# Kernel tuning notes

Hardware: AMD Instinct MI355X
Metric: run time of the kernel (lower is better)

## Reference

```python
import jax, jax.numpy as jnp
import numpy as np

D_MODEL = 1024
D_HIDDEN = 4096
N_EXPERTS = 8
N_TOKENS = 4096


def setup_inputs() -> dict:
    key = jax.random.key(0)
    ks = jax.random.split(key, 7)
    s = 0.02
    return {
        "x": jax.random.normal(ks[0], (N_TOKENS, D_MODEL), dtype=jnp.float32),
        "gate_w": jax.random.normal(ks[1], (N_EXPERTS, D_MODEL), dtype=jnp.float32) * s,
        "gate_b": jnp.zeros((N_EXPERTS,), dtype=jnp.float32),
        "w1": jax.random.normal(ks[2], (N_EXPERTS, D_MODEL, D_HIDDEN), dtype=jnp.float32) * s,
        "b1": jnp.zeros((N_EXPERTS, D_HIDDEN), dtype=jnp.float32),
        "w2": jax.random.normal(ks[3], (N_EXPERTS, D_HIDDEN, D_MODEL), dtype=jnp.float32) * s,
        "b2": jnp.zeros((N_EXPERTS, D_MODEL), dtype=jnp.float32),
    }


def reference(x, gate_w, gate_b, w1, b1, w2, b2):
    # gate: softmax over expert logits, hard top-1 routing (no prob weighting,
    # matching the torch module which writes the raw expert output back)
    gate_logits = x @ gate_w.T + gate_b                      # [N, E]
    gate_probs = jax.nn.softmax(gate_logits, axis=-1)
    top_expert = jnp.argmax(gate_probs, axis=-1)             # [N] int

    # dense all-expert MLP, then one-hot select (vectorized top-1 MoE)
    h = jax.nn.relu(jnp.einsum('nd,edh->neh', x, w1) + b1[None])  # [N, E, Dh]
    y = jnp.einsum('neh,ehd->ned', h, w2) + b2[None]              # [N, E, D]
    onehot = jax.nn.one_hot(top_expert, N_EXPERTS, dtype=x.dtype)  # [N, E]
    out = jnp.einsum('ned,ne->nd', y, onehot)                      # [N, D]
    return out
```

## Files before the change

kernel.cpp:

```cpp
#include <hip/hip_runtime.h>
#include <hip/hip_bf16.h>

#define NT 4096
#define DM 1024
#define DH 4096
#define NE 8

#define BM 128
#define BN 128
#define BK 32
#define MAXT 40
#define MAXROWS 5120
#define KSPL2 2
#define BKP 40
#define G1B (8 * 4 * MAXT)

typedef short bf16x8 __attribute__((ext_vector_type(8)));
typedef float f32x4 __attribute__((ext_vector_type(4)));
typedef float f4 __attribute__((ext_vector_type(4)));
typedef unsigned short u16x8 __attribute__((ext_vector_type(8)));

#define MI_COUNTS 0
#define MI_POFF   16
#define MI_NTILES 32
#define MI_TILEE  48
#define MI_TILER  112
#define MI_TILES0 176

#define O_BUCKET 1024ull
#define O_XB  (O_BUCKET + (size_t)NE * NT * 4)
#define O_H   (O_XB + (size_t)NT * DM * 2)
#define O_W1T (O_H + (size_t)MAXROWS * DH * 2)
#define O_W2T (O_W1T + (size_t)NE * DM * DH * 2)
#define WS_NEED (O_W2T + (size_t)NE * DH * DM * 2)
#define O_P   O_W1T

static __device__ __forceinline__ unsigned short f2bf(float f) {
  union { __hip_bfloat16 h; unsigned short u; } cv;
  cv.h = __float2bfloat16(f);
  return cv.u;
}

static __device__ __forceinline__ void gload16(const void* g, void* l) {
  __builtin_amdgcn_global_load_lds(
      (const __attribute__((address_space(1))) void*)g,
      (__attribute__((address_space(3))) void*)l, 16, 0, 0);
}

static __device__ __forceinline__ void convert_tile(
    const float* __restrict__ S, __hip_bfloat16* __restrict__ D, int K, int N,
    int k0, int n0, char* smem) {
  auto Ls = reinterpret_cast<__hip_bfloat16(*)[136]>(smem);
  const int tid = threadIdx.x;
  const int c = tid & 15, kq = tid >> 4;
  const float* src = S + (size_t)(k0 + kq * 8) * N + n0 + c * 4;
  f4 v[8];
#pragma unroll
  for (int j = 0; j < 8; ++j) v[j] = *(const f4*)(src + (size_t)j * N);
#pragma unroll
  for (int i = 0; i < 4; ++i) {
    u16x8 w;
#pragma unroll
    for (int j = 0; j < 8; ++j) w[j] = f2bf(v[j][i]);
    *(u16x8*)&Ls[c * 4 + i][kq * 8] = w;
  }
  __syncthreads();
  const int r = tid >> 2, q = tid & 3;
  __hip_bfloat16* drow = D + (size_t)(n0 + r) * K + k0 + q * 32;
#pragma unroll
  for (int u = 0; u < 4; ++u) {
    uint4 w = *(const uint4*)&Ls[r][q * 32 + u * 8];
    *(uint4*)(drow + u * 8) = w;
  }
}

static __device__ __forceinline__ void gate_body(
    const float* __restrict__ x, const float* __restrict__ gw,
    const float* __restrict__ gb, int* __restrict__ counts,
    int* __restrict__ bucket, __hip_bfloat16* __restrict__ xb, int bid) {
  const int tid = threadIdx.x;
  const int wid = tid >> 6;
  const int lane = tid & 63;
  const int t = bid * 4 + wid;

  const f4* xrow = (const f4*)(x + (size_t)t * DM);
  ushort4* xbrow = (ushort4*)(xb + (size_t)t * DM);

  double part[NE];
#pragma unroll
  for (int e = 0; e < NE; ++e) part[e] = 0.0;

#pragma unroll
  for (int q = 0; q < 4; ++q) {
    f4 v = xrow[q * 64 + lane];
    ushort4 s;
    s.x = f2bf(v[0]); s.y = f2bf(v[1]); s.z = f2bf(v[2]); s.w = f2bf(v[3]);
    xbrow[q * 64 + lane] = s;
#pragma unroll
    for (int e = 0; e < NE; ++e) {
      f4 w = ((const f4*)(gw + (size_t)e * DM))[q * 64 + lane];
      part[e] += (double)v[0] * w[0] + (double)v[1] * w[1] +
                 (double)v[2] * w[2] + (double)v[3] * w[3];
    }
  }
#pragma unroll
  for (int off = 32; off; off >>= 1) {
#pragma unroll
    for (int e = 0; e < NE; ++e) part[e] += __shfl_down(part[e], off);
  }
  if (lane == 0) {
    double best = part[0] + (double)gb[0];
    int bi = 0;
#pragma unroll
    for (int e = 1; e < NE; ++e) {
      double le = part[e] + (double)gb[e];
      if (le > best) { best = le; bi = e; }
    }
    int pos = atomicAdd(&counts[bi], 1);
    bucket[bi * NT + pos] = t;
  }
}

__global__ __launch_bounds__(256) void gate_route_kernel(
    const float* __restrict__ x, const float* __restrict__ gw,
    const float* __restrict__ gb, int* __restrict__ counts,
    int* __restrict__ bucket, __hip_bfloat16* __restrict__ xb) {
  gate_body(x, gw, gb, counts, bucket, xb, blockIdx.x);
}

__global__ __launch_bounds__(256) void cw1_kernel(
    const float* __restrict__ w1, __hip_bfloat16* __restrict__ w1t) {
  __shared__ __align__(16) char smem[17408];
  const int id = blockIdx.x;
  const int e = id & 7;
  const int rem = id >> 3;
  const int k0 = (rem & 7) * 128;
  const int n0 = (rem >> 3) * 64;
  convert_tile(w1 + (size_t)e * DM * DH, w1t + (size_t)e * DM * DH, DM, DH,
               k0, n0, smem);
}

__global__ void prefix_kernel(int* __restrict__ meta, int* __restrict__ bucket) {
  if (threadIdx.x == 0) {
    int r = 0, nt = 0;
    for (int e = 0; e < NE; ++e) {
      meta[MI_POFF + e] = r;
      const int cnt = meta[MI_COUNTS + e];
      const int T = (cnt + BM - 1) / BM;
      for (int j = 0; j < T; ++j) {
        meta[MI_TILEE + nt] = e;
        meta[MI_TILER + nt] = r + j * BM;
        meta[MI_TILES0 + nt] = j * BM;
        ++nt;
      }
      r += T * BM;
    }
    meta[MI_POFF + NE] = r;
    meta[MI_NTILES] = nt;
  }
  __syncthreads();
  for (int e = 0; e < NE; ++e) {
    const int cnt = meta[MI_COUNTS + e];
    if (cnt == 0) continue;
    const int padTo = ((cnt + BM - 1) / BM) * BM;
    const int last = bucket[e * NT + cnt - 1];
    for (int i = cnt + threadIdx.x; i < padTo; i += blockDim.x)
      bucket[e * NT + i] = last;
  }
}

template <int MODE>
static __device__ __forceinline__ void gemm_body(
    char* smem, int b, const __hip_bfloat16* __restrict__ A,
    const __hip_bfloat16* __restrict__ B, const float* __restrict__ biasAll,
    const int* __restrict__ meta, const int* __restrict__ bucket,
    void* __restrict__ Out) {
  auto As = reinterpret_cast<__hip_bfloat16(*)[BM][BK]>(smem);
  auto Bs = reinterpret_cast<__hip_bfloat16(*)[BN][BK]>(smem + 16384);

  const int xcd = b & 7;
  const int idx = b >> 3;
  int tile, ntile, kq;
  if (MODE == 0) {
    const int grp = idx / MAXT;
    tile = idx - grp * MAXT;
    ntile = xcd * 4 + grp;
    kq = 0;
  } else {
    const int grp = idx / MAXT;
    tile = idx - grp * MAXT;
    const int np = xcd * 2 + grp;
    ntile = np >> 1;
    kq = np & 1;
  }
  if (tile >= meta[MI_NTILES]) return;

  const int e = meta[MI_TILEE + tile];
  const int row0 = meta[MI_TILER + tile];
  const int s0 = meta[MI_TILES0 + tile];
  const int n0 = ntile * BN;
  const int Ktot = (MODE == 0) ? DM : DH;
  const int N = (MODE == 0) ? DH : DM;
  const int KTM = (MODE == 0) ? 32 : 64;
  const int kbase = (MODE == 0) ? 0 : kq * (DH / KSPL2);

  const int tid = threadIdx.x;
  const int lane = tid & 63;
  const int wid = tid >> 6;
  const int lr = lane >> 2, lc = lane & 3;

  const __hip_bfloat16 *aP0, *aP1;
  if (MODE == 0) {
    aP0 = A + (size_t)bucket[e * NT + s0 + 32 * wid + lr] * DM + lc * 8;
    aP1 = A + (size_t)bucket[e * NT + s0 + 32 * wid + 16 + lr] * DM + lc * 8;
  } else {
    aP0 = A + (size_t)(row0 + 32 * wid + lr) * DH + kbase + lc * 8;
    aP1 = A + (size_t)(row0 + 32 * wid + 16 + lr) * DH + kbase + lc * 8;
  }
  const __hip_bfloat16* bP0 =
      B + ((size_t)e * N + n0 + 32 * wid + lr) * Ktot + kbase + lc * 8;
  const __hip_bfloat16* bP1 = bP0 + (size_t)16 * Ktot;

  const int wm = (wid >> 1) * 64, wn = (wid & 1) * 64;
  const int fr = lane & 15, ks = lane >> 4;

  f32x4 acc[4][4];
#pragma unroll
  for (int m = 0; m < 4; ++m)
#pragma unroll
    for (int n = 0; n < 4; ++n) acc[m][n] = (f32x4){0.f, 0.f, 0.f, 0.f};

#define STAGE(bf, kt)                                  \
  do {                                                 \
    const size_t ko_ = (size_t)(kt) * BK;              \
    gload16(aP0 + ko_, &As[bf][32 * wid][0]);          \
    gload16(aP1 + ko_, &As[bf][32 * wid + 16][0]);     \
    gload16(bP0 + ko_, &Bs[bf][32 * wid][0]);          \
    gload16(bP1 + ko_, &Bs[bf][32 * wid + 16][0]);     \
  } while (0)

  STAGE(0, 0);
  __syncthreads();

  for (int kt = 0; kt < KTM; ++kt) {
    const int buf = kt & 1;
    if (kt + 1 < KTM) STAGE(buf ^ 1, kt + 1);
    bf16x8 afr[4], bfr[4];
#pragma unroll
    for (int m = 0; m < 4; ++m)
      afr[m] = *(const bf16x8*)&As[buf][wm + m * 16 + fr][ks * 8];
#pragma unroll
    for (int n = 0; n < 4; ++n)
      bfr[n] = *(const bf16x8*)&Bs[buf][wn + n * 16 + fr][ks * 8];
#pragma unroll
    for (int m = 0; m < 4; ++m)
#pragma unroll
      for (int n = 0; n < 4; ++n)
        acc[m][n] = __builtin_amdgcn_mfma_f32_16x16x32_bf16(afr[m], bfr[n],
                                                            acc[m][n], 0, 0, 0);
    __syncthreads();
  }
#undef STAGE

  if (MODE == 0) {
    const float* bias = biasAll + (size_t)e * DH;
    __hip_bfloat16* Hout = (__hip_bfloat16*)Out;
#pragma unroll
    for (int m = 0; m < 4; ++m)
#pragma unroll
      for (int r = 0; r < 4; ++r) {
        const int row = wm + m * 16 + ks * 4 + r;
        __hip_bfloat16* orow = Hout + (size_t)(row0 + row) * DH;
#pragma unroll
        for (int n = 0; n < 4; ++n) {
          const int col = n0 + wn + n * 16 + fr;
          float v = acc[m][n][r] + bias[col];
          orow[col] = __float2bfloat16(v > 0.f ? v : 0.f);
        }
      }
  } else {
    float* Pout = (float*)Out + (size_t)kq * MAXROWS * DM;
#pragma unroll
    for (int m = 0; m < 4; ++m)
#pragma unroll
      for (int r = 0; r < 4; ++r) {
        const int row = wm + m * 16 + ks * 4 + r;
        float* orow = Pout + (size_t)(row0 + row) * DM;
#pragma unroll
        for (int n = 0; n < 4; ++n) {
          const int col = n0 + wn + n * 16 + fr;
          orow[col] = acc[m][n][r];
        }
      }
  }
}

__global__ __launch_bounds__(256, 2) void gemm1_cw2_kernel(
    const __hip_bfloat16* __restrict__ xb, const __hip_bfloat16* __restrict__ w1t,
    const float* __restrict__ b1, const int* __restrict__ meta,
    const int* __restrict__ bucket, __hip_bfloat16* __restrict__ h,
    const float* __restrict__ w2, __hip_bfloat16* __restrict__ w2t) {
  __shared__ __align__(16) char smem[32768];
  const int bid = blockIdx.x;
  if (bid < G1B) {
    gemm_body<0>(smem, bid, xb, w1t, b1, meta, bucket, (void*)h);
    return;
  }
  const int id = bid - G1B;
  const int e = id >> 9, rem = id & 511;
  convert_tile(w2 + (size_t)e * DH * DM, w2t + (size_t)e * DH * DM, DH, DM,
               (rem >> 4) * 128, (rem & 15) * 64, smem);
}

__global__ __launch_bounds__(256, 2) void gemm2_kernel(
    const __hip_bfloat16* __restrict__ h, const __hip_bfloat16* __restrict__ w2t,
    const int* __restrict__ meta, const int* __restrict__ bucket,
    float* __restrict__ P) {
  __shared__ __align__(16) char smem[32768];
  gemm_body<1>(smem, blockIdx.x, h, w2t, nullptr, meta, bucket, (void*)P);
}

__global__ __launch_bounds__(256) void reduce_out_kernel(
    const float* __restrict__ P, const float* __restrict__ b2,
    const int* __restrict__ meta, const int* __restrict__ bucket,
    float* __restrict__ out) {
  const int gs = blockIdx.x;
  if (gs >= meta[MI_POFF + NE]) return;
  int e = 0;
#pragma unroll
  for (int i = 1; i < NE; ++i) e = (gs >= meta[MI_POFF + i]) ? i : e;
  const int i = gs - meta[MI_POFF + e];
  if (i >= meta[MI_COUNTS + e]) return;
  const int tok = bucket[e * NT + i];
  const int c = threadIdx.x * 4;
  float4 v = *(const float4*)(P + (size_t)gs * DM + c);
#pragma unroll
  for (int q = 1; q < KSPL2; ++q) {
    float4 p = *(const float4*)(P + ((size_t)q * MAXROWS + gs) * DM + c);
    v.x += p.x; v.y += p.y; v.z += p.z; v.w += p.w;
  }
  float4 b = *(const float4*)(b2 + (size_t)e * DM + c);
  v.x += b.x; v.y += b.y; v.z += b.z; v.w += b.w;
  *(float4*)(out + (size_t)tok * DM + c) = v;
}

template <bool RELU_BF16>
__global__ __launch_bounds__(256, 2) void moe_gemm_fallback(
    const __hip_bfloat16* __restrict__ Aall, int lda,
    const float* __restrict__ Ball, int K, int N,
    const float* __restrict__ biasAll, const int* __restrict__ counts,
    const int* __restrict__ bucket, void* __restrict__ Out, int ldo) {
  const int e = blockIdx.z;
  const int cnt = counts[e];
  const int m0 = blockIdx.y * BM;
  if (m0 >= cnt) return;
  const int n0 = blockIdx.x * BN;

  const float* Bp = Ball + (size_t)e * K * N;
  const float* bias = biasAll + (size_t)e * N;
  const int* buck = bucket + e * NT;

  __shared__ __align__(16) __hip_bfloat16 As[2][BM][BKP];
  __shared__ __align__(16) __hip_bfloat16 Bs[2][BN][BKP];

  const int tid = threadIdx.x;
  const int lane = tid & 63;
  const int wid = tid >> 6;
  const int wm = (wid >> 1) * 64;
  const int wn = (wid & 1) * 64;
  const int fr = lane & 15;
  const int ks = lane >> 4;

  const int ar = tid >> 1;
  const int ah = tid & 1;
  const int atok = buck[min(m0 + ar, cnt - 1)];
  const __hip_bfloat16* aptr = Aall + (size_t)atok * lda + ah * 16;

  const int bc = tid & 31;
  const int bk0 = (tid >> 5) * 4;

  f32x4 acc[4][4];
#pragma unroll
  for (int m = 0; m < 4; ++m)
#pragma unroll
    for (int n = 0; n < 4; ++n) acc[m][n] = (f32x4){0.f, 0.f, 0.f, 0.f};

  const int KTf = K / BK;
  uint4 ra0, ra1;
  float rb[4][4];

  {
    const uint4* p = (const uint4*)(aptr);
    ra0 = p[0]; ra1 = p[1];
    const float* bbase = Bp + (size_t)bk0 * N + n0 + bc;
#pragma unroll
    for (int i = 0; i < 4; ++i)
#pragma unroll
      for (int j = 0; j < 4; ++j) rb[i][j] = bbase[(size_t)i * N + 32 * j];
  }
  {
    *(uint4*)&As[0][ar][ah * 16] = ra0;
    *(uint4*)&As[0][ar][ah * 16 + 8] = ra1;
#pragma unroll
    for (int j = 0; j < 4; ++j) {
      ushort4 w;
      w.x = f2bf(rb[0][j]); w.y = f2bf(rb[1][j]);
      w.z = f2bf(rb[2][j]); w.w = f2bf(rb[3][j]);
      *(ushort4*)&Bs[0][bc + 32 * j][bk0] = w;
    }
  }
  __syncthreads();

  for (int kt = 0; kt < KTf; ++kt) {
    const int buf = kt & 1;
    if (kt + 1 < KTf) {
      const uint4* p = (const uint4*)(aptr + (size_t)(kt + 1) * BK);
      ra0 = p[0]; ra1 = p[1];
      const float* bbase = Bp + (size_t)((kt + 1) * BK + bk0) * N + n0 + bc;
#pragma unroll
      for (int i = 0; i < 4; ++i)
#pragma unroll
        for (int j = 0; j < 4; ++j) rb[i][j] = bbase[(size_t)i * N + 32 * j];
    }

    bf16x8 afr[4], bfr[4];
#pragma unroll
    for (int m = 0; m < 4; ++m)
      afr[m] = *(const bf16x8*)&As[buf][wm + m * 16 + fr][ks * 8];
#pragma unroll
    for (int n = 0; n < 4; ++n)
      bfr[n] = *(const bf16x8*)&Bs[buf][wn + n * 16 + fr][ks * 8];
#pragma unroll
    for (int m = 0; m < 4; ++m)
#pragma unroll
      for (int n = 0; n < 4; ++n)
        acc[m][n] = __builtin_amdgcn_mfma_f32_16x16x32_bf16(afr[m], bfr[n],
                                                            acc[m][n], 0, 0, 0);

    __syncthreads();
    if (kt + 1 < KTf) {
      *(uint4*)&As[buf ^ 1][ar][ah * 16] = ra0;
      *(uint4*)&As[buf ^ 1][ar][ah * 16 + 8] = ra1;
#pragma unroll
      for (int j = 0; j < 4; ++j) {
        ushort4 w;
        w.x = f2bf(rb[0][j]); w.y = f2bf(rb[1][j]);
        w.z = f2bf(rb[2][j]); w.w = f2bf(rb[3][j]);
        *(ushort4*)&Bs[buf ^ 1][bc + 32 * j][bk0] = w;
      }
      __syncthreads();
    }
  }

  float* outF = (float*)Out;
  __hip_bfloat16* outB = (__hip_bfloat16*)Out;
#pragma unroll
  for (int m = 0; m < 4; ++m) {
#pragma unroll
    for (int r = 0; r < 4; ++r) {
      const int row = wm + m * 16 + ks * 4 + r;
      const int slot = m0 + row;
      if (slot < cnt) {
        const int tok = buck[slot];
#pragma unroll
        for (int n = 0; n < 4; ++n) {
          const int col = n0 + wn + n * 16 + fr;
          float v = acc[m][n][r] + bias[col];
          if (RELU_BF16) {
            v = v > 0.f ? v : 0.f;
            outB[(size_t)tok * ldo + col] = __float2bfloat16(v);
          } else {
            outF[(size_t)tok * ldo + col] = v;
          }
        }
      }
    }
  }
}

extern "C" void kernel_launch(void* const* d_in, const int* in_sizes, int n_in,
                              void* d_out, int out_size, void* d_ws,
                              size_t ws_size, hipStream_t stream) {
  const float* x = (const float*)d_in[0];
  const float* gw = (const float*)d_in[1];
  const float* gb = (const float*)d_in[2];
  const float* w1 = (const float*)d_in[3];
  const float* b1 = (const float*)d_in[4];
  const float* w2 = (const float*)d_in[5];
  const float* b2 = (const float*)d_in[6];
  (void)in_sizes; (void)n_in; (void)out_size;

  char* ws = (char*)d_ws;
  int* meta = (int*)ws;
  int* counts = meta + MI_COUNTS;
  int* bucket = (int*)(ws + O_BUCKET);
  __hip_bfloat16* xb = (__hip_bfloat16*)(ws + O_XB);
  __hip_bfloat16* h = (__hip_bfloat16*)(ws + O_H);

  hipMemsetAsync(ws, 0, 1024, stream);

  if (ws_size >= WS_NEED) {
    __hip_bfloat16* w1t = (__hip_bfloat16*)(ws + O_W1T);
    __hip_bfloat16* w2t = (__hip_bfloat16*)(ws + O_W2T);
    float* P = (float*)(ws + O_P);

    gate_route_kernel<<<NT / 4, 256, 0, stream>>>(x, gw, gb, counts, bucket,
                                                  xb);
    cw1_kernel<<<4096, 256, 0, stream>>>(w1, w1t);
    prefix_kernel<<<1, 256, 0, stream>>>(meta, bucket);
    gemm1_cw2_kernel<<<G1B + 4096, 256, 0, stream>>>(
        xb, w1t, b1, meta, bucket, h, w2, w2t);
    gemm2_kernel<<<8 * 2 * MAXT, 256, 0, stream>>>(h, w2t, meta, bucket, P);
    reduce_out_kernel<<<MAXROWS, 256, 0, stream>>>(P, b2, meta, bucket,
                                                   (float*)d_out);
  } else {
    gate_route_kernel<<<NT / 4, 256, 0, stream>>>(x, gw, gb, counts, bucket,
                                                  xb);
    dim3 g1(DH / BN, NT / BM, NE);
    moe_gemm_fallback<true><<<g1, 256, 0, stream>>>(
        xb, DM, w1, DM, DH, b1, counts, bucket, (void*)h, DH);
    dim3 g2(DM / BN, NT / BM, NE);
    moe_gemm_fallback<false><<<g2, 256, 0, stream>>>(
        h, DH, w2, DH, DM, b2, counts, bucket, d_out, DM);
  }
}
```

Before: 281.3 us.

## Fuse fp32 weight conversion into GEMM B-tile loads, drop pre-transpose passes

Removes the separate kernels that converted and transposed w1 and w2 from fp32 to bf16 in workspace. The GEMMs now load fp32 weights straight from global memory into registers, convert them to bf16, and write them transposed into padded LDS, with a two-stage register prefetch. This avoids writing and re-reading the bf16 weight copies, at the cost of reading fp32 weights (twice the bytes) once per token tile. It also adds conversion ALU work and scalar global loads inside the GEMM main loop.

```diff
diff --git a/kernel.cpp b/kernel.cpp
--- a/kernel.cpp
+++ b/kernel.cpp
@@ -13,12 +13,10 @@
 #define MAXROWS 5120
 #define KSPL2 2
 #define BKP 40
-#define G1B (8 * 4 * MAXT)
 
 typedef short bf16x8 __attribute__((ext_vector_type(8)));
 typedef float f32x4 __attribute__((ext_vector_type(4)));
 typedef float f4 __attribute__((ext_vector_type(4)));
-typedef unsigned short u16x8 __attribute__((ext_vector_type(8)));
 
 #define MI_COUNTS 0
 #define MI_POFF   16
@@ -30,10 +28,8 @@
 #define O_BUCKET 1024ull
 #define O_XB  (O_BUCKET + (size_t)NE * NT * 4)
 #define O_H   (O_XB + (size_t)NT * DM * 2)
-#define O_W1T (O_H + (size_t)MAXROWS * DH * 2)
-#define O_W2T (O_W1T + (size_t)NE * DM * DH * 2)
-#define WS_NEED (O_W2T + (size_t)NE * DH * DM * 2)
-#define O_P   O_W1T
+#define O_P   (O_H + (size_t)MAXROWS * DH * 2)
+#define WS_NEED (O_P + (size_t)KSPL2 * MAXROWS * DM * 4)
 
 static __device__ __forceinline__ unsigned short f2bf(float f) {
   union { __hip_bfloat16 h; unsigned short u; } cv;
@@ -45,33 +41,6 @@
   __builtin_amdgcn_global_load_lds(
       (const __attribute__((address_space(1))) void*)g,
       (__attribute__((address_space(3))) void*)l, 16, 0, 0);
-}
-
-static __device__ __forceinline__ void convert_tile(
-    const float* __restrict__ S, __hip_bfloat16* __restrict__ D, int K, int N,
-    int k0, int n0, char* smem) {
-  auto Ls = reinterpret_cast<__hip_bfloat16(*)[136]>(smem);
-  const int tid = threadIdx.x;
-  const int c = tid & 15, kq = tid >> 4;
-  const float* src = S + (size_t)(k0 + kq * 8) * N + n0 + c * 4;
-  f4 v[8];
-#pragma unroll
-  for (int j = 0; j < 8; ++j) v[j] = *(const f4*)(src + (size_t)j * N);
-#pragma unroll
-  for (int i = 0; i < 4; ++i) {
-    u16x8 w;
-#pragma unroll
-    for (int j = 0; j < 8; ++j) w[j] = f2bf(v[j][i]);
-    *(u16x8*)&Ls[c * 4 + i][kq * 8] = w;
-  }
-  __syncthreads();
-  const int r = tid >> 2, q = tid & 3;
-  __hip_bfloat16* drow = D + (size_t)(n0 + r) * K + k0 + q * 32;
-#pragma unroll
-  for (int u = 0; u < 4; ++u) {
-    uint4 w = *(const uint4*)&Ls[r][q * 32 + u * 8];
-    *(uint4*)(drow + u * 8) = w;
-  }
 }
 
 static __device__ __forceinline__ void gate_body(
@@ -126,18 +95,6 @@
     const float* __restrict__ gb, int* __restrict__ counts,
     int* __restrict__ bucket, __hip_bfloat16* __restrict__ xb) {
   gate_body(x, gw, gb, counts, bucket, xb, blockIdx.x);
-}
-
-__global__ __launch_bounds__(256) void cw1_kernel(
-    const float* __restrict__ w1, __hip_bfloat16* __restrict__ w1t) {
-  __shared__ __align__(16) char smem[17408];
-  const int id = blockIdx.x;
-  const int e = id & 7;
-  const int rem = id >> 3;
-  const int k0 = (rem & 7) * 128;
-  const int n0 = (rem >> 3) * 64;
-  convert_tile(w1 + (size_t)e * DM * DH, w1t + (size_t)e * DM * DH, DM, DH,
-               k0, n0, smem);
 }
 
 __global__ void prefix_kernel(int* __restrict__ meta, int* __restrict__ bucket) {
@@ -170,13 +127,13 @@
 }
 
 template <int MODE>
-static __device__ __forceinline__ void gemm_body(
+static __device__ __forceinline__ void gemm_f32b(
     char* smem, int b, const __hip_bfloat16* __restrict__ A,
-    const __hip_bfloat16* __restrict__ B, const float* __restrict__ biasAll,
+    const float* __restrict__ W, const float* __restrict__ biasAll,
     const int* __restrict__ meta, const int* __restrict__ bucket,
     void* __restrict__ Out) {
   auto As = reinterpret_cast<__hip_bfloat16(*)[BM][BK]>(smem);
-  auto Bs = reinterpret_cast<__hip_bfloat16(*)[BN][BK]>(smem + 16384);
+  auto Bs = reinterpret_cast<__hip_bfloat16(*)[BN][BKP]>(smem + 16384);
 
   const int xcd = b & 7;
   const int idx = b >> 3;
@@ -199,8 +156,8 @@
   const int row0 = meta[MI_TILER + tile];
   const int s0 = meta[MI_TILES0 + tile];
   const int n0 = ntile * BN;
+  const int N = (MODE == 0) ? DH : DM;
   const int Ktot = (MODE == 0) ? DM : DH;
-  const int N = (MODE == 0) ? DH : DM;
   const int KTM = (MODE == 0) ? 32 : 64;
   const int kbase = (MODE == 0) ? 0 : kq * (DH / KSPL2);
 
@@ -217,9 +174,11 @@
     aP0 = A + (size_t)(row0 + 32 * wid + lr) * DH + kbase + lc * 8;
     aP1 = A + (size_t)(row0 + 32 * wid + 16 + lr) * DH + kbase + lc * 8;
   }
-  const __hip_bfloat16* bP0 =
-      B + ((size_t)e * N + n0 + 32 * wid + lr) * Ktot + kbase + lc * 8;
-  const __hip_bfloat16* bP1 = bP0 + (size_t)16 * Ktot;
+
+  const int bc = tid & 31;
+  const int bk0 = (tid >> 5) * 4;
+  const float* Bp = W + (size_t)e * Ktot * N + (size_t)(kbase + bk0) * N +
+                    n0 + bc;
 
   const int wm = (wid >> 1) * 64, wn = (wid & 1) * 64;
   const int fr = lane & 15, ks = lane >> 4;
@@ -230,37 +189,65 @@
 #pragma unroll
     for (int n = 0; n < 4; ++n) acc[m][n] = (f32x4){0.f, 0.f, 0.f, 0.f};
 
-#define STAGE(bf, kt)                                  \
-  do {                                                 \
-    const size_t ko_ = (size_t)(kt) * BK;              \
-    gload16(aP0 + ko_, &As[bf][32 * wid][0]);          \
-    gload16(aP1 + ko_, &As[bf][32 * wid + 16][0]);     \
-    gload16(bP0 + ko_, &Bs[bf][32 * wid][0]);          \
-    gload16(bP1 + ko_, &Bs[bf][32 * wid + 16][0]);     \
+  float rb[4][4];
+
+#define BLOAD(kt)                                                     \
+  do {                                                                \
+    const float* bbase = Bp + (size_t)(kt) * BK * N;                  \
+    _Pragma("unroll") for (int i = 0; i < 4; ++i)                     \
+        _Pragma("unroll") for (int j = 0; j < 4; ++j)                 \
+            rb[i][j] = bbase[(size_t)i * N + 32 * j];                 \
   } while (0)
 
-  STAGE(0, 0);
+#define BWRITE(bf)                                                    \
+  do {                                                                \
+    _Pragma("unroll") for (int j = 0; j < 4; ++j) {                   \
+      ushort4 w;                                                      \
+      w.x = f2bf(rb[0][j]); w.y = f2bf(rb[1][j]);                     \
+      w.z = f2bf(rb[2][j]); w.w = f2bf(rb[3][j]);                     \
+      *(ushort4*)&Bs[bf][bc + 32 * j][bk0] = w;                       \
+    }                                                                 \
+  } while (0)
+
+#define ASTAGE(bf, kt)                                                \
+  do {                                                                \
+    gload16(aP0 + (size_t)(kt) * BK, &As[bf][32 * wid][0]);           \
+    gload16(aP1 + (size_t)(kt) * BK, &As[bf][32 * wid + 16][0]);      \
+  } while (0)
+
+#define COMPUTE(bf)                                                          \
+  do {                                                                       \
+    bf16x8 afr[4], bfr[4];                                                   \
+    _Pragma("unroll") for (int m = 0; m < 4; ++m)                            \
+        afr[m] = *(const bf16x8*)&As[bf][wm + m * 16 + fr][ks * 8];          \
+    _Pragma("unroll") for (int n = 0; n < 4; ++n)                            \
+        bfr[n] = *(const bf16x8*)&Bs[bf][wn + n * 16 + fr][ks * 8];          \
+    _Pragma("unroll") for (int m = 0; m < 4; ++m)                            \
+        _Pragma("unroll") for (int n = 0; n < 4; ++n)                        \
+            acc[m][n] = __builtin_amdgcn_mfma_f32_16x16x32_bf16(             \
+                afr[m], bfr[n], acc[m][n], 0, 0, 0);                         \
+  } while (0)
+
+  BLOAD(0);
+  ASTAGE(0, 0);
+  BWRITE(0);
+  BLOAD(1);
   __syncthreads();
 
   for (int kt = 0; kt < KTM; ++kt) {
     const int buf = kt & 1;
-    if (kt + 1 < KTM) STAGE(buf ^ 1, kt + 1);
-    bf16x8 afr[4], bfr[4];
-#pragma unroll
-    for (int m = 0; m < 4; ++m)
-      afr[m] = *(const bf16x8*)&As[buf][wm + m * 16 + fr][ks * 8];
-#pragma unroll
-    for (int n = 0; n < 4; ++n)
-      bfr[n] = *(const bf16x8*)&Bs[buf][wn + n * 16 + fr][ks * 8];
-#pragma unroll
-    for (int m = 0; m < 4; ++m)
-#pragma unroll
-      for (int n = 0; n < 4; ++n)
-        acc[m][n] = __builtin_amdgcn_mfma_f32_16x16x32_bf16(afr[m], bfr[n],
-                                                            acc[m][n], 0, 0, 0);
+    if (kt + 1 < KTM) {
+      BWRITE(buf ^ 1);
+      ASTAGE(buf ^ 1, kt + 1);
+      if (kt + 2 < KTM) BLOAD(kt + 2);
+    }
+    COMPUTE(buf);
     __syncthreads();
   }
-#undef STAGE
+#undef BLOAD
+#undef BWRITE
+#undef ASTAGE
+#undef COMPUTE
 
   if (MODE == 0) {
     const float* bias = biasAll + (size_t)e * DH;
@@ -295,29 +282,20 @@
   }
 }
 
-__global__ __launch_bounds__(256, 2) void gemm1_cw2_kernel(
-    const __hip_bfloat16* __restrict__ xb, const __hip_bfloat16* __restrict__ w1t,
+__global__ __launch_bounds__(256, 2) void gemm1f_kernel(
+    const __hip_bfloat16* __restrict__ xb, const float* __restrict__ w1,
     const float* __restrict__ b1, const int* __restrict__ meta,
-    const int* __restrict__ bucket, __hip_bfloat16* __restrict__ h,
-    const float* __restrict__ w2, __hip_bfloat16* __restrict__ w2t) {
-  __shared__ __align__(16) char smem[32768];
-  const int bid = blockIdx.x;
-  if (bid < G1B) {
-    gemm_body<0>(smem, bid, xb, w1t, b1, meta, bucket, (void*)h);
-    return;
-  }
-  const int id = bid - G1B;
-  const int e = id >> 9, rem = id & 511;
-  convert_tile(w2 + (size_t)e * DH * DM, w2t + (size_t)e * DH * DM, DH, DM,
-               (rem >> 4) * 128, (rem & 15) * 64, smem);
-}
-
-__global__ __launch_bounds__(256, 2) void gemm2_kernel(
-    const __hip_bfloat16* __restrict__ h, const __hip_bfloat16* __restrict__ w2t,
+    const int* __restrict__ bucket, __hip_bfloat16* __restrict__ h) {
+  __shared__ __align__(16) char smem[36864];
+  gemm_f32b<0>(smem, blockIdx.x, xb, w1, b1, meta, bucket, (void*)h);
+}
+
+__global__ __launch_bounds__(256, 2) void gemm2f_kernel(
+    const __hip_bfloat16* __restrict__ h, const float* __restrict__ w2,
     const int* __restrict__ meta, const int* __restrict__ bucket,
     float* __restrict__ P) {
-  __shared__ __align__(16) char smem[32768];
-  gemm_body<1>(smem, blockIdx.x, h, w2t, nullptr, meta, bucket, (void*)P);
+  __shared__ __align__(16) char smem[36864];
+  gemm_f32b<1>(smem, blockIdx.x, h, w2, nullptr, meta, bucket, (void*)P);
 }
 
 __global__ __launch_bounds__(256) void reduce_out_kernel(
@@ -496,21 +474,17 @@
   int* bucket = (int*)(ws + O_BUCKET);
   __hip_bfloat16* xb = (__hip_bfloat16*)(ws + O_XB);
   __hip_bfloat16* h = (__hip_bfloat16*)(ws + O_H);
+  float* P = (float*)(ws + O_P);
 
   hipMemsetAsync(ws, 0, 1024, stream);
 
   if (ws_size >= WS_NEED) {
-    __hip_bfloat16* w1t = (__hip_bfloat16*)(ws + O_W1T);
-    __hip_bfloat16* w2t = (__hip_bfloat16*)(ws + O_W2T);
-    float* P = (float*)(ws + O_P);
-
     gate_route_kernel<<<NT / 4, 256, 0, stream>>>(x, gw, gb, counts, bucket,
                                                   xb);
-    cw1_kernel<<<4096, 256, 0, stream>>>(w1, w1t);
     prefix_kernel<<<1, 256, 0, stream>>>(meta, bucket);
-    gemm1_cw2_kernel<<<G1B + 4096, 256, 0, stream>>>(
-        xb, w1t, b1, meta, bucket, h, w2, w2t);
-    gemm2_kernel<<<8 * 2 * MAXT, 256, 0, stream>>>(h, w2t, meta, bucket, P);
+    gemm1f_kernel<<<8 * 4 * MAXT, 256, 0, stream>>>(xb, w1, b1, meta, bucket,
+                                                    h);
+    gemm2f_kernel<<<8 * 2 * MAXT, 256, 0, stream>>>(h, w2, meta, bucket, P);
     reduce_out_kernel<<<MAXROWS, 256, 0, stream>>>(P, b2, meta, bucket,
                                                    (float*)d_out);
   } else {
```

Result: faster. 265.7 us (-5.5%).
